# Kernel optimization log

Hardware: AMD Instinct MI355X
Metric: run time of the kernel (lower is better)

Reference implementation:

```python
import math
import jax, jax.numpy as jnp
import numpy as np

D_MODEL = 512
N_HEADS = 8
HEAD_DIM = D_MODEL // N_HEADS
B, T = 2, 2048


def _sinusoid_pe(T, d):
    # Transformer-XL relative sinusoids for distances -(T-1)..(T-1) -> (2T-1, d)
    pos = jnp.arange(-(T - 1), T, dtype=jnp.float32)
    div = jnp.exp(2.0 * jnp.arange(d // 2, dtype=jnp.float32) * (-math.log(10000.0) / d))
    terms = pos[:, None] * div[None, :]
    pe = jnp.zeros((2 * T - 1, d), dtype=jnp.float32)
    pe = pe.at[:, 0::2].set(jnp.sin(terms)).at[:, 1::2].set(jnp.cos(terms))
    return pe


def _relative_shift(s):
    # s: (B, H, T, 2T-1) -> shifted (B, H, T, T)
    b, h, t, l = s.shape
    s = jnp.pad(s, ((0, 0), (0, 0), (0, 0), (1, 0)))        # (B,H,T,2T)
    s = s.reshape(b, h, l + 1, t)[:, :, 1:, :].reshape(b, h, t, l)
    return s[:, :, :, :t]


def setup_inputs() -> dict:
    key = jax.random.key(0)
    ks = jax.random.split(key, 12)
    sw = 1.0 / math.sqrt(D_MODEL)
    su = math.sqrt(6.0 / (N_HEADS + HEAD_DIM))  # xavier_uniform bound
    inp = {
        "x": jax.random.normal(ks[0], (B, T, D_MODEL), jnp.float32),
        "mask": jnp.ones((B, 1, T, T), jnp.int32),
        "Wq": jax.random.normal(ks[1], (D_MODEL, D_MODEL), jnp.float32) * sw,
        "bq": jax.random.normal(ks[2], (D_MODEL,), jnp.float32) * 0.01,
        "Wv": jax.random.normal(ks[3], (D_MODEL, D_MODEL), jnp.float32) * sw,
        "bv": jax.random.normal(ks[4], (D_MODEL,), jnp.float32) * 0.01,
        "Wkc": jax.random.normal(ks[5], (D_MODEL, D_MODEL), jnp.float32) * sw,
        "bkc": jax.random.normal(ks[6], (D_MODEL,), jnp.float32) * 0.01,
        "Wkl": jax.random.normal(ks[7], (D_MODEL, D_MODEL), jnp.float32) * sw,
        "bkl": jax.random.normal(ks[8], (D_MODEL,), jnp.float32) * 0.01,
        "u": jax.random.uniform(ks[9], (N_HEADS, HEAD_DIM), jnp.float32, -su, su),
        "v": jax.random.uniform(ks[10], (N_HEADS, HEAD_DIM), jnp.float32, -su, su),
    }
    return inp


def reference(x, mask, Wq, bq, Wv, bv, Wkc, bkc, Wkl, bkl, u, v):
    b, t, d = x.shape
    h, hd = u.shape
    pe = _sinusoid_pe(t, d)                                   # (2T-1, D)
    q = (x @ Wq.T + bq).reshape(b, t, h, hd)                  # (B,T,H,hd)
    val = (x @ Wv.T + bv).reshape(b, t, h, hd)                # (B,T,H,hd)
    kc = (x @ Wkc.T + bkc).reshape(b, t, h, hd)               # (B,T,H,hd)
    kl = (pe @ Wkl.T + bkl).reshape(2 * t - 1, h, hd)         # (2T-1,H,hd)
    ac = jnp.einsum('bqhd,bkhd->bhqk', q + u, kc)             # content score
    bd = jnp.einsum('bqhd,lhd->bhql', q + v, kl)              # position score
    bd = _relative_shift(bd)                                  # (B,H,T,T)
    attn = (ac + bd) / math.sqrt(hd)
    attn = jnp.where(mask == 0, -jnp.inf, attn)
    p = jax.nn.softmax(attn, axis=-1)
    out = jnp.einsum('bhqk,bkhd->bqhd', p, val)
    return out.reshape(b, t, d)
```

## Files before the change

### kernel.cpp

```cpp
#include <hip/hip_runtime.h>
#include <hip/hip_bf16.h>

#define BB 2
#define TT 2048
#define DD 512
#define HH 8
#define HD 64

typedef __bf16 bf16;
typedef __bf16 bf16x8 __attribute__((ext_vector_type(8)));
typedef float f32x4 __attribute__((ext_vector_type(4)));
typedef unsigned int u32;

#define SCL 0.1803368801111204f

static __device__ __forceinline__ f32x4 mfma16(bf16x8 a, bf16x8 b, f32x4 c) {
  return __builtin_amdgcn_mfma_f32_16x16x32_bf16(a, b, c, 0, 0, 0);
}
static __device__ __forceinline__ u32 cvtpk(float lo, float hi) {
  u32 r; asm("v_cvt_pk_bf16_f32 %0, %1, %2" : "=v"(r) : "v"(lo), "v"(hi)); return r;
}
#define PERM(a, b, s) __builtin_amdgcn_perm((a), (b), (s))

#define GL16(gp, lp) __builtin_amdgcn_global_load_lds( \
    (const __attribute__((address_space(1))) unsigned int*)(gp), \
    (__attribute__((address_space(3))) unsigned int*)(lp), 16, 0, 0)

__global__ __launch_bounds__(256) void prep_kernel(
    const float* __restrict__ x,
    const float* __restrict__ Wq, const float* __restrict__ Wkc,
    const float* __restrict__ Wv, const float* __restrict__ Wkl,
    bf16* __restrict__ xb, bf16* __restrict__ wqb, bf16* __restrict__ wkcb,
    bf16* __restrict__ wvb, bf16* __restrict__ wklb, bf16* __restrict__ peb)
{
  int bid = blockIdx.x;
  int tid = threadIdx.x;
  if (bid < 1536) {
    const float* src; bf16* dst; int off;
    if (bid < 1024) { src = x; dst = xb; off = bid * 2048 + tid * 8; }
    else {
      int g = (bid - 1024) >> 7;
      src = (g == 0) ? Wq : (g == 1) ? Wkc : (g == 2) ? Wv : Wkl;
      dst = (g == 0) ? wqb : (g == 1) ? wkcb : (g == 2) ? wvb : wklb;
      off = ((bid - 1024) & 127) * 2048 + tid * 8;
    }
    float4 v0 = *(const float4*)(src + off);
    float4 v1 = *(const float4*)(src + off + 4);
    bf16 o[8] = {(bf16)v0.x,(bf16)v0.y,(bf16)v0.z,(bf16)v0.w,
                 (bf16)v1.x,(bf16)v1.y,(bf16)v1.z,(bf16)v1.w};
    *(bf16x8*)(dst + off) = *(bf16x8*)o;
  } else {
    int p = (bid - 1536) * 2048 + tid * 8;
    int row = p >> 8;
    int pc = p & 255;
    float pos = (float)(row - (TT - 1));
    bool valid = (row < 2 * TT - 1);
#pragma unroll
    for (int j = 0; j < 8; ++j) {
      int i = pc + j;
      float sv = 0.f, cv = 0.f;
      if (valid) {
        float div = exp2f((float)i * -0.051905124764638574f);
        float t = pos * div;
        __sincosf(t, &sv, &cv);
      }
      peb[(size_t)row * DD + 2 * i]     = (bf16)sv;
      peb[(size_t)row * DD + 2 * i + 1] = (bf16)cv;
    }
  }
}

__global__ __launch_bounds__(256) void gemm_all(
    const bf16* __restrict__ xb, const bf16* __restrict__ peb,
    const bf16* __restrict__ wq, const bf16* __restrict__ wkc,
    const bf16* __restrict__ wv, const bf16* __restrict__ wkl,
    const float* __restrict__ bq, const float* __restrict__ bkc,
    const float* __restrict__ bv, const float* __restrict__ bkl,
    const float* __restrict__ uu, const float* __restrict__ vv,
    bf16* __restrict__ qu, bf16* __restrict__ qv, bf16* __restrict__ kc,
    bf16* __restrict__ vt, bf16* __restrict__ kl)
{
  __shared__ __align__(16) bf16 Al[2][128 * 64];
  __shared__ __align__(16) bf16 Bl[2][128 * 64];

  int bid = blockIdx.x;
  int j = bid >> 3;
  int n_tile = ((bid & 7) << 1) | (j >> 5);
  int m_tile = j & 31;
  int mode = n_tile >> 2;
  int n0 = (n_tile & 3) * 128;
  int m0 = m_tile * 128;

  int tid = threadIdx.x;
  int w = tid >> 6, lane = tid & 63;
  int lr = lane & 15, lg = lane >> 4;
  int wr = w >> 1, wc = w & 1;

  const bf16* A = (mode == 3) ? peb : xb;
  const bf16* W = (mode == 0) ? wq : (mode == 1) ? wkc : (mode == 2) ? wv : wkl;
  const float* bias = (mode == 0) ? bq : (mode == 1) ? bkc : (mode == 2) ? bv : bkl;

  int srow = w * 32 + (lane >> 3);
  int schunk = (lane & 7) ^ (lane >> 3);
  const bf16* Abase = A + (size_t)(m0 + srow) * DD + 8 * schunk;
  const bf16* Wbase = W + (size_t)(n0 + srow) * DD + 8 * schunk;

  auto STAGE = [&](int buf, int k0) {
#pragma unroll
    for (int i = 0; i < 4; ++i) {
      GL16(Abase + (size_t)i * 8 * DD + k0, &Al[buf][(w * 32 + i * 8) * 64]);
      GL16(Wbase + (size_t)i * 8 * DD + k0, &Bl[buf][(w * 32 + i * 8) * 64]);
    }
  };

  f32x4 acc[4][4];
#pragma unroll
  for (int tm = 0; tm < 4; ++tm)
#pragma unroll
    for (int tn = 0; tn < 4; ++tn) acc[tm][tn] = (f32x4){0.f, 0.f, 0.f, 0.f};

  STAGE(0, 0);
  __syncthreads();

#pragma unroll 1
  for (int kk = 0; kk < 8; ++kk) {
    int cur = kk & 1;
    if (kk < 7) STAGE(cur ^ 1, (kk + 1) * 64);
    const bf16* Ab = Al[cur];
    const bf16* Bb = Bl[cur];
#pragma unroll
    for (int s = 0; s < 2; ++s) {
      bf16x8 af[4], bfr[4];
#pragma unroll
      for (int t = 0; t < 4; ++t) {
        int arow = wr * 64 + 16 * t + lr;
        af[t]  = *(const bf16x8*)(Ab + arow * 64 + 8 * ((4 * s + lg) ^ (lr & 7)));
        int brow = wc * 64 + 16 * t + lr;
        bfr[t] = *(const bf16x8*)(Bb + brow * 64 + 8 * ((4 * s + lg) ^ (lr & 7)));
      }
#pragma unroll
      for (int tm = 0; tm < 4; ++tm)
#pragma unroll
        for (int tn = 0; tn < 4; ++tn)
          acc[tm][tn] = mfma16(af[tm], bfr[tn], acc[tm][tn]);
    }
    __syncthreads();
  }

#pragma unroll
  for (int tn = 0; tn < 4; ++tn) {
    int n = n0 + wc * 64 + 16 * tn + lr;
    float bn = bias[n];
    int h = n >> 6, d = n & 63;
    float ua = 0.f, va = 0.f;
    if (mode == 0) { ua = uu[h * HD + d]; va = vv[h * HD + d]; }
#pragma unroll
    for (int tm = 0; tm < 4; ++tm) {
#pragma unroll
      for (int r = 0; r < 4; ++r) {
        int m = m0 + wr * 64 + 16 * tm + lg * 4 + r;
        float val = acc[tm][tn][r] + bn;
        if (mode == 0) {
          int bb = m >> 11, tp = m & (TT - 1);
          size_t idx = ((size_t)(bb * HH + h) * TT + tp) * HD + d;
          qu[idx] = (bf16)((val + ua) * SCL);
          qv[idx] = (bf16)((val + va) * SCL);
        } else if (mode == 1) {
          int bb = m >> 11, tp = m & (TT - 1);
          kc[((size_t)(bb * HH + h) * TT + tp) * HD + d] = (bf16)val;
        } else if (mode == 2) {
          int bb = m >> 11, tp = m & (TT - 1);
          vt[((size_t)(bb * HH + h) * HD + d) * TT + tp] = (bf16)val;
        } else {
          kl[((size_t)h * 4096 + m) * HD + d] = (bf16)val;
        }
      }
    }
  }
}

__global__ __launch_bounds__(512) void attn_kernel(
    const bf16* __restrict__ QU, const bf16* __restrict__ QV,
    const bf16* __restrict__ KC, const bf16* __restrict__ VT,
    const bf16* __restrict__ KL, float* __restrict__ out)
{
  __shared__ __align__(16) char smem[86016];
  bf16* kcL0 = (bf16*)smem;
  bf16* kcL1 = (bf16*)(smem + 8192);
  bf16* vtL0 = (bf16*)(smem + 16384);
  bf16* vtL1 = (bf16*)(smem + 24576);
  bf16* kq0 = (bf16*)(smem + 32768);
  bf16* kq1 = (bf16*)(smem + 40960);
  bf16* kq2 = (bf16*)(smem + 49152);
  bf16* kq3 = (bf16*)(smem + 57344);
  bf16* Pl  = (bf16*)(smem + 65536);

  int bid = blockIdx.x;
  int xcd = bid & 7, j = bid >> 3;
  int g = (xcd << 1) | (j >> 4);
  int qt = j & 15;
  int b = g >> 3, h = g & 7;
  int q0 = qt * 128;

  int tid = threadIdx.x;
  int w = tid >> 6;
  int lane = tid & 63;
  int lr = lane & 15, lg = lane >> 4;
  int qg = w & 3, kh = w >> 2;
  int qw0 = q0 + qg * 32;

  int rsub = lane >> 3, chunk = lane & 7;
  int srow = w * 8 + rsub;
  int csrc = chunk ^ rsub;
  int ldst = w * 512;

  const bf16* qu_bh = QU + (size_t)(b * HH + h) * TT * HD;
  const bf16* qv_bh = QV + (size_t)(b * HH + h) * TT * HD;
  const bf16* kc_bh = KC + (size_t)(b * HH + h) * TT * HD;
  const bf16* vt_bh = VT + (size_t)(b * HH + h) * HD * TT;
  const bf16* kl_h  = KL + (size_t)h * 4096 * HD;

  bf16x8 quf[2][2], qvf[2][2];
#pragma unroll
  for (int sub = 0; sub < 2; ++sub)
#pragma unroll
    for (int s = 0; s < 2; ++s) {
      quf[sub][s] = *(const bf16x8*)(qu_bh + (size_t)(qw0 + 16 * sub + lr) * HD + 32 * s + 8 * lg);
      qvf[sub][s] = *(const bf16x8*)(qv_bh + (size_t)(qw0 + 16 * sub + lr) * HD + 32 * s + 8 * lg);
    }

  int B0 = 1920 - q0;

  GL16(kc_bh + (size_t)srow * 64 + csrc * 8, kcL0 + ldst);
  GL16(vt_bh + (size_t)srow * TT + csrc * 8, vtL0 + ldst);
  GL16(kl_h + (size_t)(B0 + srow) * 64 + csrc * 8, kq0 + ldst);
  GL16(kl_h + (size_t)(B0 + 64 + srow) * 64 + csrc * 8, kq1 + ldst);
  GL16(kl_h + (size_t)(B0 + 128 + srow) * 64 + csrc * 8, kq2 + ldst);
  __syncthreads();

  bf16* kcCur = kcL0; bf16* kcNxt = kcL1;
  bf16* vtCur = vtL0; bf16* vtNxt = vtL1;
  bf16* kp0 = kq0; bf16* kp1 = kq1; bf16* kp2 = kq2; bf16* kp3 = kq3;

  f32x4 accO[2][4];
#pragma unroll
  for (int sub = 0; sub < 2; ++sub)
#pragma unroll
    for (int t = 0; t < 4; ++t) accO[sub][t] = (f32x4){0.f, 0.f, 0.f, 0.f};
  float plsum[2][4] = {{0.f,0.f,0.f,0.f},{0.f,0.f,0.f,0.f}};
  int wrow0u = 96 + 32 * kh - 32 * qg;
  int pchb = lr & 7;

  u32 pat[4]; int srcl[4];
#pragma unroll
  for (int r = 0; r < 4; ++r) {
    int row = lg * 4 + r;
    pat[r]  = (lr <= row) ? 0x05040000u : 0x07060000u;
    srcl[r] = (lane & 48) | ((15 + lr - row) & 15);
  }

#pragma unroll 1
  for (int kt = 0; kt < 32; ++kt) {
    if (kt < 31) {
      int k1 = (kt + 1) * 64;
      GL16(kc_bh + (size_t)(k1 + srow) * 64 + csrc * 8, kcNxt + ldst);
      GL16(vt_bh + (size_t)srow * TT + k1 + csrc * 8, vtNxt + ldst);
      GL16(kl_h + (size_t)(B0 + 64 * kt + 192 + srow) * 64 + csrc * 8, kp3 + ldst);
    }

    f32x4 S[2][2], a[2][3];
    __builtin_amdgcn_s_setprio(1);
#pragma unroll
    for (int t = 0; t < 2; ++t) {
      int row = 32 * kh + 16 * t + lr;
      f32x4 a0 = (f32x4){0.f,0.f,0.f,0.f}, a1 = (f32x4){0.f,0.f,0.f,0.f};
#pragma unroll
      for (int s = 0; s < 2; ++s) {
        int pch = (4 * s + lg) ^ pchb;
        bf16x8 kb = *(const bf16x8*)(&kcCur[row * 64 + pch * 8]);
        a0 = mfma16(quf[0][s], kb, a0);
        a1 = mfma16(quf[1][s], kb, a1);
      }
      S[0][t] = a0; S[1][t] = a1;
    }

    {
      bf16x8 kb4[4][2];
#pragma unroll
      for (int t = 0; t < 4; ++t) {
        int rel = wrow0u + 16 * t + lr;
        const bf16* pb = (rel & 128) ? kp2 : ((rel & 64) ? kp1 : kp0);
        int off = rel & 63;
#pragma unroll
        for (int s = 0; s < 2; ++s) {
          int pch = (4 * s + lg) ^ pchb;
          kb4[t][s] = *(const bf16x8*)(&pb[off * 64 + pch * 8]);
        }
      }
#pragma unroll
      for (int sub = 0; sub < 2; ++sub)
#pragma unroll
        for (int i = 0; i < 3; ++i) {
          f32x4 acc = (f32x4){0.f,0.f,0.f,0.f};
          int t = i + 1 - sub;
#pragma unroll
          for (int s = 0; s < 2; ++s) acc = mfma16(qvf[sub][s], kb4[t][s], acc);
          a[sub][i] = acc;
        }
    }
    __builtin_amdgcn_s_setprio(0);

    float p[2][2][4];
#pragma unroll
    for (int sub = 0; sub < 2; ++sub)
#pragma unroll
      for (int t = 0; t < 2; ++t)
#pragma unroll
        for (int r = 0; r < 4; ++r) {
          u32 pk = cvtpk(a[sub][t][r], a[sub][t + 1][r]);
          u32 gb = __shfl(pk, srcl[r], 64);
          float wv = __builtin_bit_cast(float, PERM(gb, 0u, pat[r]));
          float e = __builtin_exp2f(S[sub][t][r] + wv);
          p[sub][t][r] = e;
          plsum[sub][r] += e;
        }

#pragma unroll
    for (int sub = 0; sub < 2; ++sub)
#pragma unroll
      for (int r = 0; r < 4; ++r) {
        Pl[((w * 2 + sub) * 16 + 4 * lg + r) * 40 + lr]      = (bf16)p[sub][0][r];
        Pl[((w * 2 + sub) * 16 + 4 * lg + r) * 40 + 16 + lr] = (bf16)p[sub][1][r];
      }
    {
      bf16x8 pa0 = *(const bf16x8*)(&Pl[((w * 2 + 0) * 16 + lr) * 40 + 8 * lg]);
      bf16x8 pa1 = *(const bf16x8*)(&Pl[((w * 2 + 1) * 16 + lr) * 40 + 8 * lg]);
      __builtin_amdgcn_s_setprio(1);
#pragma unroll
      for (int t = 0; t < 4; ++t) {
        int row = 16 * t + lr;
        int pch = (4 * kh + lg) ^ pchb;
        bf16x8 vb = *(const bf16x8*)(&vtCur[row * 64 + pch * 8]);
        accO[0][t] = mfma16(pa0, vb, accO[0][t]);
        accO[1][t] = mfma16(pa1, vb, accO[1][t]);
      }
      __builtin_amdgcn_s_setprio(0);
    }

    __syncthreads();

    bf16* tmp;
    tmp = kcCur; kcCur = kcNxt; kcNxt = tmp;
    tmp = vtCur; vtCur = vtNxt; vtNxt = tmp;
    tmp = kp0; kp0 = kp1; kp1 = kp2; kp2 = kp3; kp3 = tmp;
  }

#pragma unroll
  for (int msk = 1; msk < 16; msk <<= 1)
#pragma unroll
    for (int sub = 0; sub < 2; ++sub)
#pragma unroll
      for (int r = 0; r < 4; ++r) plsum[sub][r] += __shfl_xor(plsum[sub][r], msk, 64);

  float* rO = (float*)(smem + 32768);
  float* rS = (float*)(smem + 32768 + 34816);
  if (kh == 1) {
#pragma unroll
    for (int sub = 0; sub < 2; ++sub)
#pragma unroll
      for (int r = 0; r < 4; ++r) {
        int qloc = qg * 32 + 16 * sub + 4 * lg + r;
#pragma unroll
        for (int t = 0; t < 4; ++t) rO[qloc * 68 + 16 * t + lr] = accO[sub][t][r];
        if (lr == 0) rS[qloc] = plsum[sub][r];
      }
  }
  __syncthreads();
  if (kh == 0) {
#pragma unroll
    for (int sub = 0; sub < 2; ++sub)
#pragma unroll
      for (int r = 0; r < 4; ++r) {
        int qloc = qg * 32 + 16 * sub + 4 * lg + r;
        float inv = 1.f / (plsum[sub][r] + rS[qloc]);
        int q = qw0 + 16 * sub + 4 * lg + r;
        float* op = out + (size_t)(b * TT + q) * DD + h * HD;
#pragma unroll
        for (int t = 0; t < 4; ++t)
          op[16 * t + lr] = (accO[sub][t][r] + rO[qloc * 68 + 16 * t + lr]) * inv;
      }
  }
}

extern "C" void kernel_launch(void* const* d_in, const int* in_sizes, int n_in,
                              void* d_out, int out_size, void* d_ws, size_t ws_size,
                              hipStream_t stream) {
  const float* x   = (const float*)d_in[0];
  const float* Wq  = (const float*)d_in[2];
  const float* bq  = (const float*)d_in[3];
  const float* Wv  = (const float*)d_in[4];
  const float* bv  = (const float*)d_in[5];
  const float* Wkc = (const float*)d_in[6];
  const float* bkc = (const float*)d_in[7];
  const float* Wkl = (const float*)d_in[8];
  const float* bkl = (const float*)d_in[9];
  const float* u   = (const float*)d_in[10];
  const float* v   = (const float*)d_in[11];
  float* out = (float*)d_out;

  char* ws = (char*)d_ws;
  const size_t MB = 1024 * 1024;
  bf16* xb   = (bf16*)(ws + 0);
  bf16* peb  = (bf16*)(ws + 4 * MB);
  bf16* wqb  = (bf16*)(ws + 8 * MB);
  bf16* wkcb = (bf16*)(ws + 8 * MB + 512 * 1024);
  bf16* wvb  = (bf16*)(ws + 9 * MB);
  bf16* wklb = (bf16*)(ws + 9 * MB + 512 * 1024);
  bf16* qu   = (bf16*)(ws + 10 * MB);
  bf16* qv   = (bf16*)(ws + 14 * MB);
  bf16* kc   = (bf16*)(ws + 18 * MB);
  bf16* vt   = (bf16*)(ws + 22 * MB);
  bf16* kl   = (bf16*)(ws + 26 * MB);

  prep_kernel<<<2048, 256, 0, stream>>>(x, Wq, Wkc, Wv, Wkl,
                                        xb, wqb, wkcb, wvb, wklb, peb);
  gemm_all<<<512, 256, 0, stream>>>(xb, peb, wqb, wkcb, wvb, wklb,
                                    bq, bkc, bv, bkl, u, v,
                                    qu, qv, kc, vt, kl);
  attn_kernel<<<256, 512, 0, stream>>>(qu, qv, kc, vt, kl, out);
}
```

Baseline: 96.97 us.

## Split attention key range across two blocks and add reduction kernel

Each attention block now handles half the key range (1024 keys), doubling the grid from 256 to 512 blocks so more CUs are occupied on the chip. Partial unnormalized outputs are stored in bf16 and partial row sums in fp32 to workspace, and a new reduce kernel combines the two halves and normalizes. The P staging buffer in LDS is halved by reusing one slot per wave for both sub-tiles. This adds an extra kernel launch, extra global traffic and bf16 rounding of the partial accumulators.

```diff
diff --git a/kernel.cpp b/kernel.cpp
--- a/kernel.cpp
+++ b/kernel.cpp
@@ -182,9 +182,9 @@
 __global__ __launch_bounds__(512) void attn_kernel(
     const bf16* __restrict__ QU, const bf16* __restrict__ QV,
     const bf16* __restrict__ KC, const bf16* __restrict__ VT,
-    const bf16* __restrict__ KL, float* __restrict__ out)
+    const bf16* __restrict__ KL, bf16* __restrict__ pacc, float* __restrict__ psum)
 {
-  __shared__ __align__(16) char smem[86016];
+  __shared__ __align__(16) char smem[75776];
   bf16* kcL0 = (bf16*)smem;
   bf16* kcL1 = (bf16*)(smem + 8192);
   bf16* vtL0 = (bf16*)(smem + 16384);
@@ -197,10 +197,12 @@
 
   int bid = blockIdx.x;
   int xcd = bid & 7, j = bid >> 3;
-  int g = (xcd << 1) | (j >> 4);
-  int qt = j & 15;
+  int g = (xcd << 1) | (j >> 5);
+  int qt = (j >> 1) & 15;
+  int kh2 = j & 1;
   int b = g >> 3, h = g & 7;
   int q0 = qt * 128;
+  int k00 = kh2 * 1024;
 
   int tid = threadIdx.x;
   int w = tid >> 6;
@@ -229,10 +231,10 @@
       qvf[sub][s] = *(const bf16x8*)(qv_bh + (size_t)(qw0 + 16 * sub + lr) * HD + 32 * s + 8 * lg);
     }
 
-  int B0 = 1920 - q0;
-
-  GL16(kc_bh + (size_t)srow * 64 + csrc * 8, kcL0 + ldst);
-  GL16(vt_bh + (size_t)srow * TT + csrc * 8, vtL0 + ldst);
+  int B0 = 1920 - q0 + k00;
+
+  GL16(kc_bh + (size_t)(k00 + srow) * 64 + csrc * 8, kcL0 + ldst);
+  GL16(vt_bh + (size_t)srow * TT + k00 + csrc * 8, vtL0 + ldst);
   GL16(kl_h + (size_t)(B0 + srow) * 64 + csrc * 8, kq0 + ldst);
   GL16(kl_h + (size_t)(B0 + 64 + srow) * 64 + csrc * 8, kq1 + ldst);
   GL16(kl_h + (size_t)(B0 + 128 + srow) * 64 + csrc * 8, kq2 + ldst);
@@ -260,9 +262,9 @@
   }
 
 #pragma unroll 1
-  for (int kt = 0; kt < 32; ++kt) {
-    if (kt < 31) {
-      int k1 = (kt + 1) * 64;
+  for (int kt = 0; kt < 16; ++kt) {
+    if (kt < 15) {
+      int k1 = k00 + (kt + 1) * 64;
       GL16(kc_bh + (size_t)(k1 + srow) * 64 + csrc * 8, kcNxt + ldst);
       GL16(vt_bh + (size_t)srow * TT + k1 + csrc * 8, vtNxt + ldst);
       GL16(kl_h + (size_t)(B0 + 64 * kt + 192 + srow) * 64 + csrc * 8, kp3 + ldst);
@@ -325,24 +327,25 @@
           plsum[sub][r] += e;
         }
 
-#pragma unroll
-    for (int sub = 0; sub < 2; ++sub)
+    bf16x8 pa[2];
+#pragma unroll
+    for (int sub = 0; sub < 2; ++sub) {
 #pragma unroll
       for (int r = 0; r < 4; ++r) {
-        Pl[((w * 2 + sub) * 16 + 4 * lg + r) * 40 + lr]      = (bf16)p[sub][0][r];
-        Pl[((w * 2 + sub) * 16 + 4 * lg + r) * 40 + 16 + lr] = (bf16)p[sub][1][r];
-      }
+        Pl[(w * 16 + 4 * lg + r) * 40 + lr]      = (bf16)p[sub][0][r];
+        Pl[(w * 16 + 4 * lg + r) * 40 + 16 + lr] = (bf16)p[sub][1][r];
+      }
+      pa[sub] = *(const bf16x8*)(&Pl[(w * 16 + lr) * 40 + 8 * lg]);
+    }
     {
-      bf16x8 pa0 = *(const bf16x8*)(&Pl[((w * 2 + 0) * 16 + lr) * 40 + 8 * lg]);
-      bf16x8 pa1 = *(const bf16x8*)(&Pl[((w * 2 + 1) * 16 + lr) * 40 + 8 * lg]);
       __builtin_amdgcn_s_setprio(1);
 #pragma unroll
       for (int t = 0; t < 4; ++t) {
         int row = 16 * t + lr;
         int pch = (4 * kh + lg) ^ pchb;
         bf16x8 vb = *(const bf16x8*)(&vtCur[row * 64 + pch * 8]);
-        accO[0][t] = mfma16(pa0, vb, accO[0][t]);
-        accO[1][t] = mfma16(pa1, vb, accO[1][t]);
+        accO[0][t] = mfma16(pa[0], vb, accO[0][t]);
+        accO[1][t] = mfma16(pa[1], vb, accO[1][t]);
       }
       __builtin_amdgcn_s_setprio(0);
     }
@@ -382,13 +385,44 @@
 #pragma unroll
       for (int r = 0; r < 4; ++r) {
         int qloc = qg * 32 + 16 * sub + 4 * lg + r;
-        float inv = 1.f / (plsum[sub][r] + rS[qloc]);
-        int q = qw0 + 16 * sub + 4 * lg + r;
-        float* op = out + (size_t)(b * TT + q) * DD + h * HD;
 #pragma unroll
         for (int t = 0; t < 4; ++t)
-          op[16 * t + lr] = (accO[sub][t][r] + rO[qloc * 68 + 16 * t + lr]) * inv;
-      }
+          pacc[(size_t)bid * 8192 + qloc * 64 + 16 * t + lr] =
+              (bf16)(accO[sub][t][r] + rO[qloc * 68 + 16 * t + lr]);
+        if (lr == 0) psum[bid * 128 + qloc] = plsum[sub][r] + rS[qloc];
+      }
+  }
+}
+
+__global__ __launch_bounds__(256) void reduce_kernel(
+    const bf16* __restrict__ pacc, const float* __restrict__ psum,
+    float* __restrict__ out)
+{
+  int pb = blockIdx.x;
+  int g = pb >> 4, qt = pb & 15;
+  int xcd = g >> 1;
+  int jA = ((g & 1) << 5) | (qt << 1);
+  int bidA = xcd + 8 * jA;
+  int bidB = bidA + 8;
+  int b = g >> 3, h = g & 7;
+
+  int tid = threadIdx.x;
+  int qr = tid >> 1;
+  int d0 = (tid & 1) * 32;
+
+  const bf16* pA = pacc + (size_t)bidA * 8192 + qr * 64 + d0;
+  const bf16* pB = pacc + (size_t)bidB * 8192 + qr * 64 + d0;
+  float inv = 1.f / (psum[bidA * 128 + qr] + psum[bidB * 128 + qr]);
+
+  int q = qt * 128 + qr;
+  float* op = out + (size_t)(b * TT + q) * DD + h * HD + d0;
+#pragma unroll
+  for (int i0 = 0; i0 < 32; i0 += 8) {
+    bf16x8 av = *(const bf16x8*)(pA + i0);
+    bf16x8 bv = *(const bf16x8*)(pB + i0);
+#pragma unroll
+    for (int i = 0; i < 8; ++i)
+      op[i0 + i] = ((float)av[i] + (float)bv[i]) * inv;
   }
 }
 
@@ -421,11 +455,14 @@
   bf16* kc   = (bf16*)(ws + 18 * MB);
   bf16* vt   = (bf16*)(ws + 22 * MB);
   bf16* kl   = (bf16*)(ws + 26 * MB);
+  bf16* pacc = (bf16*)(ws + 30 * MB);
+  float* psum = (float*)(ws + 38 * MB);
 
   prep_kernel<<<2048, 256, 0, stream>>>(x, Wq, Wkc, Wv, Wkl,
                                         xb, wqb, wkcb, wvb, wklb, peb);
   gemm_all<<<512, 256, 0, stream>>>(xb, peb, wqb, wkcb, wvb, wklb,
                                     bq, bkc, bv, bkl, u, v,
                                     qu, qv, kc, vt, kl);
-  attn_kernel<<<256, 512, 0, stream>>>(qu, qv, kc, vt, kl, out);
-}
+  attn_kernel<<<512, 512, 0, stream>>>(qu, qv, kc, vt, kl, pacc, psum);
+  reduce_kernel<<<256, 256, 0, stream>>>(pacc, psum, out);
+}
```

New measurement: 106.2 us. 1.1x slower.
